# Kernel optimization log

Measured on AMD Instinct MI355X. Metric: run time of the kernel, lower is better.

## Reference

```python
import jax, jax.numpy as jnp
import numpy as np

P = 16; IMG = 800; GRID = IMG // P; NP = GRID * GRID  # 2500 patches
D = P * P * 3  # 768
H = 8; HD = D // H; FF = 2048; L = 2; B = 2
NM = NP // 2; NV = NP - NM  # 1250 / 1250


def _ln(x, g, b):
    m = x.mean(-1, keepdims=True)
    v = ((x - m) ** 2).mean(-1, keepdims=True)
    return (x - m) * jax.lax.rsqrt(v + 1e-5) * g + b


def _block(x, qkv_w, qkv_b, out_w, out_b, w1, b1, w2, b2, g1, be1, g2, be2):
    # pre-LN-free MAE block: attn -> add&norm -> FFN -> add&norm (dropout in eval = identity)
    Bb, N, _ = x.shape
    qkv = (x @ qkv_w + qkv_b).reshape(Bb, N, 3, H, HD)
    q, k, v = qkv[:, :, 0], qkv[:, :, 1], qkv[:, :, 2]  # [B,N,H,HD]
    scores = jnp.einsum('bnhd,bmhd->bhnm', q, k) / np.float32(np.sqrt(HD))
    w = jax.nn.softmax(scores, axis=-1)
    ao = jnp.einsum('bhnm,bmhd->bnhd', w, v).reshape(Bb, N, D) @ out_w + out_b
    x = _ln(x + ao, g1, be1)
    f = jax.nn.relu(x @ w1 + b1) @ w2 + b2
    return _ln(x + f, g2, be2)


def _patchify(x):
    Bb = x.shape[0]
    # torch unfold(2,P,P).unfold(3,P,P) -> [B,C,h,w,p,p] -> [B,h*w,C*p*p]
    return x.reshape(Bb, 3, GRID, P, GRID, P).transpose(0, 2, 4, 1, 3, 5).reshape(Bb, NP, D)


def setup_inputs() -> dict:
    key = jax.random.key(0)
    ks = jax.random.split(key, 32)
    inp = {}
    inp['x'] = jax.random.normal(ks[0], (B, 3, IMG, IMG), jnp.float32)
    perm = jax.vmap(lambda k: jax.random.permutation(k, NP))(jax.random.split(ks[1], B))
    inp['visible_idx'] = perm[:, NM:].astype(jnp.int32)  # perm order, like torch
    inp['masked_idx'] = perm[:, :NM].astype(jnp.int32)
    c = [2]
    def nx(shape, s=0.02):
        k = ks[c[0]]; c[0] += 1
        return jax.random.normal(k, shape, jnp.float32) * s
    for p in ['enc', 'dec']:
        inp[p + '_qkv_w'] = nx((L, D, 3 * D)); inp[p + '_qkv_b'] = jnp.zeros((L, 3 * D), jnp.float32)
        inp[p + '_out_w'] = nx((L, D, D));     inp[p + '_out_b'] = jnp.zeros((L, D), jnp.float32)
        inp[p + '_w1'] = nx((L, D, FF));       inp[p + '_b1'] = jnp.zeros((L, FF), jnp.float32)
        inp[p + '_w2'] = nx((L, FF, D));       inp[p + '_b2'] = jnp.zeros((L, D), jnp.float32)
        inp[p + '_g1'] = jnp.ones((L, D), jnp.float32);  inp[p + '_be1'] = jnp.zeros((L, D), jnp.float32)
        inp[p + '_g2'] = jnp.ones((L, D), jnp.float32);  inp[p + '_be2'] = jnp.zeros((L, D), jnp.float32)
    inp['out_w'] = nx((D, D)); inp['out_b'] = jnp.zeros((D,), jnp.float32)
    inp['mask_token'] = nx((D,))
    inp['enc_pos'] = nx((NV, D))
    inp['dec_pos'] = nx((NP, D))
    return inp


def reference(x, visible_idx, masked_idx,
              enc_qkv_w, enc_qkv_b, enc_out_w, enc_out_b, enc_w1, enc_b1, enc_w2, enc_b2,
              enc_g1, enc_be1, enc_g2, enc_be2,
              dec_qkv_w, dec_qkv_b, dec_out_w, dec_out_b, dec_w1, dec_b1, dec_w2, dec_b2,
              dec_g1, dec_be1, dec_g2, dec_be2,
              out_w, out_b, mask_token, enc_pos, dec_pos):
    patches = _patchify(x)                                    # [B,NP,D]
    b_ix = jnp.arange(B)[:, None]
    vis = patches[b_ix, visible_idx]                          # [B,NV,D] in perm order
    h = vis + enc_pos[None]
    for i in range(L):
        h = _block(h, enc_qkv_w[i], enc_qkv_b[i], enc_out_w[i], enc_out_b[i],
                   enc_w1[i], enc_b1[i], enc_w2[i], enc_b2[i],
                   enc_g1[i], enc_be1[i], enc_g2[i], enc_be2[i])
    # torch: full_sequence[mask==0] = visible_patches (row-major positions <- perm-order rows)
    vis_pos = jnp.sort(visible_idx, axis=1)
    full = jnp.broadcast_to(mask_token, (B, NP, D))           # masked positions = mask_token
    full = full.at[b_ix, vis_pos].set(h)
    h = full + dec_pos[None]
    for i in range(L):
        h = _block(h, dec_qkv_w[i], dec_qkv_b[i], dec_out_w[i], dec_out_b[i],
                   dec_w1[i], dec_b1[i], dec_w2[i], dec_b2[i],
                   dec_g1[i], dec_be1[i], dec_g2[i], dec_be2[i])
    return h @ out_w + out_b                                  # [B,NP,D]
```

## Files before the change

### kernel.cpp

```cpp
#include <hip/hip_runtime.h>
#include <cstdint>
#include <cstddef>


#define NBATCH  2
#define NPATCH  2500
#define NVIS    1250
#define DMODEL  768
#define NHEAD   8
#define HDIM    96
#define FFDIM   2048
#define NPADV   2560

typedef __attribute__((ext_vector_type(8))) short bf16x8;
typedef __attribute__((ext_vector_type(4))) float f32x4;

__device__ __forceinline__ short f2bf(float f){
  union { float f; unsigned u; } x; x.f = f;
  unsigned r = x.u + 0x7fffu + ((x.u >> 16) & 1u);
  return (short)(r >> 16);
}

__device__ __forceinline__ void async_copy16(void* lds, const void* g){
  __builtin_amdgcn_global_load_lds(
      (const __attribute__((address_space(1))) unsigned int*)g,
      (__attribute__((address_space(3))) unsigned int*)lds, 16, 0, 0);
}

struct TJob { const float* src; short* dst; int K; int N; int tile_base; int tiles_x; };
struct TJobs { TJob j[17]; };

__global__ __launch_bounds__(256) void transpose_all_kernel(TJobs jobs){
  int bid = blockIdx.x;
  int ji = 0;
  #pragma unroll
  for (int k=1;k<17;k++) if (bid >= jobs.j[k].tile_base) ji = k;
  TJob jb = jobs.j[ji];
  int lt = bid - jb.tile_base;
  int tx = lt % jb.tiles_x, ty = lt / jb.tiles_x;
  __shared__ float tile[32][33];
  int lx = threadIdx.x & 31, ly = threadIdx.x >> 5;
  #pragma unroll
  for (int r=0;r<4;r++)
    tile[ly + r*8][lx] = jb.src[(size_t)(ty*32 + ly + r*8)*jb.N + tx*32 + lx];
  __syncthreads();
  #pragma unroll
  for (int r=0;r<4;r++)
    jb.dst[(size_t)(tx*32 + ly + r*8)*jb.K + ty*32 + lx] = f2bf(tile[lx][ly + r*8]);
}

template<int MODE>
__global__ __launch_bounds__(256) void gemm_kernel(const short* __restrict__ A,
    const short* __restrict__ Wt, const float* __restrict__ bias,
    short* __restrict__ Cb, float* __restrict__ Cf, int M, int Nc, int K){
  __shared__ short ldsA[128*64];
  __shared__ short ldsB[128*64];
  const int t = threadIdx.x, w = t>>6, ln = t&63;
  const int m0 = blockIdx.x*128, n0 = blockIdx.y*128;
  const int wr = (w>>1)*64, wc = (w&1)*64;
  const f32x4 fz = {0.f,0.f,0.f,0.f};
  f32x4 acc[4][4];
  #pragma unroll
  for (int mi=0;mi<4;mi++)
    #pragma unroll
    for (int ni=0;ni<4;ni++) acc[mi][ni] = fz;
  const int nkt = K >> 6;
  for (int kt=0; kt<nkt; kt++){
    #pragma unroll
    for (int c=0;c<4;c++){
      int chunk = c*256 + t;
      int row = chunk>>3, seg = chunk&7, sgs = seg ^ (row&7);
      int gm = m0 + row; if (gm >= M) gm = M-1;
      async_copy16((char*)ldsA + c*4096 + w*1024, A  + (size_t)gm*K      + kt*64 + sgs*8);
      async_copy16((char*)ldsB + c*4096 + w*1024, Wt + (size_t)(n0+row)*K + kt*64 + sgs*8);
    }
    __syncthreads();
    #pragma unroll
    for (int ks=0;ks<2;ks++){
      bf16x8 af[4], bfr[4];
      #pragma unroll
      for (int mi=0;mi<4;mi++){
        int r = wr + mi*16 + (ln&15);
        int d = ks*4 + (ln>>4);
        af[mi]  = *(const bf16x8*)((const char*)ldsA + r*128 + ((d^(r&7))*16));
        int cc = wc + mi*16 + (ln&15);
        bfr[mi] = *(const bf16x8*)((const char*)ldsB + cc*128 + ((d^(cc&7))*16));
      }
      #pragma unroll
      for (int mi=0;mi<4;mi++)
        #pragma unroll
        for (int ni=0;ni<4;ni++)
          acc[mi][ni] = __builtin_amdgcn_mfma_f32_16x16x32_bf16(af[mi], bfr[ni], acc[mi][ni], 0,0,0);
    }
    __syncthreads();
  }
  float bv[4];
  #pragma unroll
  for (int ni=0;ni<4;ni++) bv[ni] = bias[n0 + wc + ni*16 + (ln&15)];
  #pragma unroll
  for (int mi=0;mi<4;mi++){
    #pragma unroll
    for (int j=0;j<4;j++){
      int gr = m0 + wr + mi*16 + (ln>>4)*4 + j;
      if (gr < M){
        #pragma unroll
        for (int ni=0;ni<4;ni++){
          float v = acc[mi][ni][j] + bv[ni];
          if (MODE==2) v = fmaxf(v, 0.f);
          int gc = n0 + wc + ni*16 + (ln&15);
          if (MODE==1) Cf[(size_t)gr*Nc + gc] = v;
          else         Cb[(size_t)gr*Nc + gc] = f2bf(v);
        }
      }
    }
  }
}

__global__ __launch_bounds__(256) void vtrans_kernel(const short* __restrict__ qkv,
    short* __restrict__ vt, int N){
  int bh = blockIdx.z;
  int b = bh >> 3, h = bh & 7;
  int n0 = blockIdx.x*32, hd0 = blockIdx.y*32;
  __shared__ short tile[32][33];
  int lx = threadIdx.x & 31, ly = threadIdx.x >> 5;
  #pragma unroll
  for (int r=0;r<4;r++){
    int n = n0 + ly + r*8;
    short val = 0;
    if (n < N) val = qkv[(size_t)(b*N+n)*2304 + 1536 + h*96 + hd0 + lx];
    tile[ly+r*8][lx] = val;
  }
  __syncthreads();
  #pragma unroll
  for (int r=0;r<4;r++){
    int hd = hd0 + ly + r*8, n = n0 + lx;
    vt[(size_t)(bh*96 + hd)*NPADV + n] = tile[lx][ly+r*8];
  }
}

__global__ __launch_bounds__(256) void attn_kernel(const short* __restrict__ qkv,
    const short* __restrict__ vt, short* __restrict__ ao, int N, int NT){
  __shared__ short Qs[64*104];
  __shared__ short Ks[64*104];
  __shared__ short Vs[96*72];
  __shared__ float Ps[4*16*68];
  const int t = threadIdx.x, w = t>>6, ln = t&63;
  const int bh = blockIdx.y, b = bh >> 3, h = bh & 7;
  const int q0 = blockIdx.x * 64;
  const float scale = 0.1020620726159658f;
  #pragma unroll
  for (int i=0;i<3;i++){
    int chunk = i*256 + t; int row = chunk/12, cs = chunk - row*12;
    int gn = q0 + row; if (gn >= N) gn = N-1;
    const short* gp = qkv + (size_t)(b*N+gn)*2304 + h*96 + cs*8;
    *(bf16x8*)&Qs[row*104 + cs*8] = *(const bf16x8*)gp;
  }
  __syncthreads();
  bf16x8 qf[3];
  #pragma unroll
  for (int ks=0;ks<3;ks++)
    qf[ks] = *(const bf16x8*)&Qs[(w*16 + (ln&15))*104 + (ks*4 + (ln>>4))*8];
  const f32x4 fz = {0.f,0.f,0.f,0.f};
  f32x4 o[6];
  #pragma unroll
  for (int g=0; g<6; g++) o[g] = fz;
  float mrun[4] = {-1e30f,-1e30f,-1e30f,-1e30f};
  float srun[4] = {0.f,0.f,0.f,0.f};
  for (int kt=0; kt<NT; kt++){
    int n0 = kt*64;
    #pragma unroll
    for (int i=0;i<3;i++){
      int chunk = i*256 + t; int row = chunk/12, cs = chunk - row*12;
      int gn = n0 + row; if (gn >= N) gn = N-1;
      const short* gp = qkv + (size_t)(b*N+gn)*2304 + 768 + h*96 + cs*8;
      *(bf16x8*)&Ks[row*104 + cs*8] = *(const bf16x8*)gp;
    }
    #pragma unroll
    for (int i=0;i<3;i++){
      int chunk = i*256 + t; int row = chunk>>3, seg = chunk&7;
      const short* gp = vt + (size_t)(bh*96 + row)*NPADV + n0 + seg*8;
      *(bf16x8*)&Vs[row*72 + seg*8] = *(const bf16x8*)gp;
    }
    __syncthreads();
    f32x4 s[4];
    #pragma unroll
    for (int tt=0;tt<4;tt++){
      f32x4 sc = fz;
      #pragma unroll
      for (int ks=0;ks<3;ks++){
        bf16x8 kb = *(const bf16x8*)&Ks[(tt*16 + (ln&15))*104 + (ks*4 + (ln>>4))*8];
        sc = __builtin_amdgcn_mfma_f32_16x16x32_bf16(qf[ks], kb, sc, 0,0,0);
      }
      int col = n0 + tt*16 + (ln&15);
      float msk = (col < N) ? 0.f : -1e30f;
      #pragma unroll
      for (int j=0;j<4;j++) s[tt][j] = sc[j]*scale + msk;
    }
    #pragma unroll
    for (int j=0;j<4;j++){
      float mx = fmaxf(fmaxf(s[0][j], s[1][j]), fmaxf(s[2][j], s[3][j]));
      #pragma unroll
      for (int d=1; d<16; d<<=1) mx = fmaxf(mx, __shfl_xor(mx, d));
      float mnew = fmaxf(mrun[j], mx);
      float alpha = __expf(mrun[j] - mnew);
      mrun[j] = mnew;
      float ps = 0.f;
      #pragma unroll
      for (int tt=0;tt<4;tt++){ float pv = __expf(s[tt][j] - mnew); s[tt][j] = pv; ps += pv; }
      #pragma unroll
      for (int d=1; d<16; d<<=1) ps += __shfl_xor(ps, d);
      srun[j] = srun[j]*alpha + ps;
      #pragma unroll
      for (int g=0; g<6; g++) o[g][j] *= alpha;
    }
    #pragma unroll
    for (int tt=0;tt<4;tt++)
      #pragma unroll
      for (int j=0;j<4;j++)
        Ps[(w*16 + (ln>>4)*4 + j)*68 + tt*16 + (ln&15)] = s[tt][j];
    #pragma unroll
    for (int ks2=0; ks2<2; ks2++){
      const float* pr = &Ps[(w*16 + (ln&15))*68 + ks2*32 + (ln>>4)*8];
      f32x4 p0 = *(const f32x4*)pr;
      f32x4 p1 = *(const f32x4*)(pr+4);
      bf16x8 pa;
      #pragma unroll
      for (int j=0;j<4;j++){ pa[j] = f2bf(p0[j]); pa[4+j] = f2bf(p1[j]); }
      #pragma unroll
      for (int g=0; g<6; g++){
        bf16x8 vb = *(const bf16x8*)&Vs[(g*16 + (ln&15))*72 + (ks2*4 + (ln>>4))*8];
        o[g] = __builtin_amdgcn_mfma_f32_16x16x32_bf16(pa, vb, o[g], 0,0,0);
      }
    }
    __syncthreads();
  }
  float inv[4];
  #pragma unroll
  for (int j=0;j<4;j++) inv[j] = 1.f / srun[j];
  #pragma unroll
  for (int g=0; g<6; g++)
    #pragma unroll
    for (int j=0;j<4;j++){
      int qr = q0 + w*16 + (ln>>4)*4 + j;
      if (qr < N)
        ao[(size_t)(b*N+qr)*768 + h*96 + g*16 + (ln&15)] = f2bf(o[g][j]*inv[j]);
    }
}

__global__ __launch_bounds__(256) void ln_kernel(const float* __restrict__ xin,
    const float* __restrict__ add, const float* __restrict__ g,
    const float* __restrict__ be, float* __restrict__ xo, short* __restrict__ xob){
  int row = blockIdx.x, t = threadIdx.x;
  float e[3]; float s = 0.f;
  #pragma unroll
  for (int k=0;k<3;k++){
    size_t off = (size_t)row*768 + t + k*256;
    e[k] = xin[off] + add[off]; s += e[k];
  }
  #pragma unroll
  for (int d=32; d; d>>=1) s += __shfl_xor(s, d);
  __shared__ float red[8];
  if ((t&63)==0) red[t>>6] = s;
  __syncthreads();
  float mean = (red[0]+red[1]+red[2]+red[3]) * (1.f/768.f);
  float vs = 0.f;
  #pragma unroll
  for (int k=0;k<3;k++){ float dd = e[k]-mean; vs += dd*dd; }
  #pragma unroll
  for (int d=32; d; d>>=1) vs += __shfl_xor(vs, d);
  if ((t&63)==0) red[4 + (t>>6)] = vs;
  __syncthreads();
  float rstd = rsqrtf((red[4]+red[5]+red[6]+red[7]) * (1.f/768.f) + 1e-5f);
  #pragma unroll
  for (int k=0;k<3;k++){
    int c = t + k*256;
    size_t off = (size_t)row*768 + c;
    float ov = (e[k]-mean)*rstd*g[c] + be[c];
    xo[off] = ov; xob[off] = f2bf(ov);
  }
}

__global__ __launch_bounds__(256) void patchify_kernel(const float* __restrict__ x,
    const int* __restrict__ vis, const float* __restrict__ enc_pos,
    float* __restrict__ xe, short* __restrict__ xeb){
  int b = blockIdx.y, i = blockIdx.x;
  int pidx = vis[b*NVIS + i];
  int gy = pidx / 50, gx = pidx - gy*50;
  #pragma unroll
  for (int k=0;k<3;k++){
    int d = threadIdx.x + k*256;
    int c = d >> 8, rr = d & 255, py = rr >> 4, px = rr & 15;
    float v = x[(((size_t)b*3 + c)*800 + gy*16 + py)*800 + gx*16 + px]
            + enc_pos[(size_t)i*768 + d];
    size_t off = (size_t)(b*NVIS + i)*768 + d;
    xe[off] = v; xeb[off] = f2bf(v);
  }
}

__global__ __launch_bounds__(256) void rank_kernel(const int* __restrict__ vis,
    int* __restrict__ rnk){
  int b = blockIdx.y; int i = blockIdx.x*256 + threadIdx.x;
  if (i >= NVIS) return;
  int p = vis[b*NVIS + i]; int c = 0;
  for (int j=0;j<NVIS;j++) c += (vis[b*NVIS + j] < p) ? 1 : 0;
  rnk[b*NVIS + i] = c;
}

__global__ __launch_bounds__(256) void dec_init_kernel(const float* __restrict__ mask_token,
    const float* __restrict__ dec_pos, float* __restrict__ xd, short* __restrict__ xdb){
  int row = blockIdx.x;
  int p = row % NPATCH;
  #pragma unroll
  for (int k=0;k<3;k++){
    int c = threadIdx.x + k*256;
    float v = mask_token[c] + dec_pos[(size_t)p*768 + c];
    size_t off = (size_t)row*768 + c;
    xd[off] = v; xdb[off] = f2bf(v);
  }
}

__global__ __launch_bounds__(256) void scatter_kernel(const int* __restrict__ vis,
    const int* __restrict__ rnk, const float* __restrict__ xe,
    const float* __restrict__ dec_pos, float* __restrict__ xd, short* __restrict__ xdb){
  int b = blockIdx.y, i = blockIdx.x;
  int p = vis[b*NVIS+i]; int r = rnk[b*NVIS+i];
  #pragma unroll
  for (int k=0;k<3;k++){
    int c = threadIdx.x + k*256;
    float v = xe[(size_t)(b*NVIS + r)*768 + c] + dec_pos[(size_t)p*768 + c];
    size_t off = (size_t)(b*NPATCH + p)*768 + c;
    xd[off] = v; xdb[off] = f2bf(v);
  }
}

static void run_block(hipStream_t stream, float* xf, short* xb, int M, int N, int NT,
                      const short* wqkvT, const float* qkv_b, const short* woutT,
                      const float* out_b, const short* w1T, const float* b1,
                      const short* w2T, const float* b2,
                      const float* g1, const float* be1, const float* g2, const float* be2,
                      short* qkvb, short* vt, short* aob, short* ffnb, float* tmp){
  int mt = (M + 127)/128;
  gemm_kernel<0><<<dim3(mt, 18), 256, 0, stream>>>(xb, wqkvT, qkv_b, qkvb, nullptr, M, 2304, 768);
  vtrans_kernel<<<dim3(NT*2, 3, 16), 256, 0, stream>>>(qkvb, vt, N);
  attn_kernel<<<dim3(NT, 16), 256, 0, stream>>>(qkvb, vt, aob, N, NT);
  gemm_kernel<1><<<dim3(mt, 6), 256, 0, stream>>>(aob, woutT, out_b, nullptr, tmp, M, 768, 768);
  ln_kernel<<<M, 256, 0, stream>>>(xf, tmp, g1, be1, xf, xb);
  gemm_kernel<2><<<dim3(mt, 16), 256, 0, stream>>>(xb, w1T, b1, ffnb, nullptr, M, 2048, 768);
  gemm_kernel<1><<<dim3(mt, 6), 256, 0, stream>>>(ffnb, w2T, b2, nullptr, tmp, M, 768, 2048);
  ln_kernel<<<M, 256, 0, stream>>>(xf, tmp, g2, be2, xf, xb);
}

extern "C" void kernel_launch(void* const* d_in, const int* in_sizes, int n_in,
                              void* d_out, int out_size, void* d_ws, size_t ws_size,
                              hipStream_t stream){
  const float* x        = (const float*)d_in[0];
  const int*   vis      = (const int*)d_in[1];
  const float* eqkv_w   = (const float*)d_in[3];
  const float* eqkv_b   = (const float*)d_in[4];
  const float* eout_w   = (const float*)d_in[5];
  const float* eout_b   = (const float*)d_in[6];
  const float* ew1      = (const float*)d_in[7];
  const float* eb1      = (const float*)d_in[8];
  const float* ew2      = (const float*)d_in[9];
  const float* eb2      = (const float*)d_in[10];
  const float* eg1      = (const float*)d_in[11];
  const float* ebe1     = (const float*)d_in[12];
  const float* eg2      = (const float*)d_in[13];
  const float* ebe2     = (const float*)d_in[14];
  const float* dqkv_w   = (const float*)d_in[15];
  const float* dqkv_b   = (const float*)d_in[16];
  const float* dout_w   = (const float*)d_in[17];
  const float* dout_b   = (const float*)d_in[18];
  const float* dw1      = (const float*)d_in[19];
  const float* db1      = (const float*)d_in[20];
  const float* dw2      = (const float*)d_in[21];
  const float* db2      = (const float*)d_in[22];
  const float* dg1      = (const float*)d_in[23];
  const float* dbe1     = (const float*)d_in[24];
  const float* dg2      = (const float*)d_in[25];
  const float* dbe2     = (const float*)d_in[26];
  const float* fout_w   = (const float*)d_in[27];
  const float* fout_b   = (const float*)d_in[28];
  const float* mask_tok = (const float*)d_in[29];
  const float* enc_posp = (const float*)d_in[30];
  const float* dec_posp = (const float*)d_in[31];

  char* p = (char*)d_ws;
  auto alloc = [&](size_t bytes)->char*{ char* r = p; p += (bytes + 255) & ~(size_t)255; return r; };

  const float* qkvw_s[2] = {eqkv_w, dqkv_w};
  const float* outw_s[2] = {eout_w, dout_w};
  const float* w1_s[2]   = {ew1, dw1};
  const float* w2_s[2]   = {ew2, dw2};

  short *wq[2][2], *wo[2][2], *w1t[2][2], *w2t[2][2];
  TJobs jobs; int jidx = 0; int tbase = 0;
  auto addJob = [&](const float* src, short* dst, int K, int N){
    jobs.j[jidx].src = src; jobs.j[jidx].dst = dst; jobs.j[jidx].K = K; jobs.j[jidx].N = N;
    jobs.j[jidx].tile_base = tbase; jobs.j[jidx].tiles_x = N/32;
    tbase += (K/32)*(N/32); jidx++;
  };
  for (int s=0;s<2;s++)
    for (int i=0;i<2;i++){
      wq[s][i]  = (short*)alloc((size_t)2304*768*2);
      addJob(qkvw_s[s] + (size_t)i*768*2304, wq[s][i], 768, 2304);
      wo[s][i]  = (short*)alloc((size_t)768*768*2);
      addJob(outw_s[s] + (size_t)i*768*768, wo[s][i], 768, 768);
      w1t[s][i] = (short*)alloc((size_t)2048*768*2);
      addJob(w1_s[s] + (size_t)i*768*2048, w1t[s][i], 768, 2048);
      w2t[s][i] = (short*)alloc((size_t)768*2048*2);
      addJob(w2_s[s] + (size_t)i*2048*768, w2t[s][i], 2048, 768);
    }
  short* wfin = (short*)alloc((size_t)768*768*2);
  addJob(fout_w, wfin, 768, 768);
  int total_tiles = tbase;

  float* xe   = (float*)alloc((size_t)2500*768*4);
  short* xeb  = (short*)alloc((size_t)2500*768*2);
  float* xd   = (float*)alloc((size_t)5000*768*4);
  short* xdb  = (short*)alloc((size_t)5000*768*2);
  short* qkvb = (short*)alloc((size_t)5000*2304*2);
  short* vt   = (short*)alloc((size_t)16*96*NPADV*2);
  short* aob  = (short*)alloc((size_t)5000*768*2);
  short* ffnb = (short*)alloc((size_t)5000*2048*2);
  float* tmp  = (float*)alloc((size_t)5000*768*4);
  int*   rnk  = (int*)alloc((size_t)2*NVIS*4);

  transpose_all_kernel<<<total_tiles, 256, 0, stream>>>(jobs);
  patchify_kernel<<<dim3(NVIS, NBATCH), 256, 0, stream>>>(x, vis, enc_posp, xe, xeb);
  rank_kernel<<<dim3((NVIS+255)/256, NBATCH), 256, 0, stream>>>(vis, rnk);

  for (int i=0;i<2;i++)
    run_block(stream, xe, xeb, 2500, 1250, 20,
              wq[0][i], eqkv_b + i*2304, wo[0][i], eout_b + i*768,
              w1t[0][i], eb1 + i*2048, w2t[0][i], eb2 + i*768,
              eg1 + i*768, ebe1 + i*768, eg2 + i*768, ebe2 + i*768,
              qkvb, vt, aob, ffnb, tmp);

  dec_init_kernel<<<NBATCH*NPATCH, 256, 0, stream>>>(mask_tok, dec_posp, xd, xdb);
  scatter_kernel<<<dim3(NVIS, NBATCH), 256, 0, stream>>>(vis, rnk, xe, dec_posp, xd, xdb);

  for (int i=0;i<2;i++)
    run_block(stream, xd, xdb, 5000, 2500, 40,
              wq[1][i], dqkv_b + i*2304, wo[1][i], dout_b + i*768,
              w1t[1][i], db1 + i*2048, w2t[1][i], db2 + i*768,
              dg1 + i*768, dbe1 + i*768, dg2 + i*768, dbe2 + i*768,
              qkvb, vt, aob, ffnb, tmp);

  gemm_kernel<1><<<dim3(40, 6), 256, 0, stream>>>(xdb, wfin, fout_b, nullptr,
                                                  (float*)d_out, 5000, 768, 768);
}
```

Before: 1.197 ms.

## Restructure attention kernel with async swizzled LDS loads and lazy softmax rescale

Rewrites the flash-attention inner loop. Q is loaded straight into registers, and K/V tiles are copied with async global-to-LDS copies into an XOR-swizzled layout to avoid bank conflicts. The softmax now uses exp2 with a folded log2e scale, rescales the running max only when it grows past a threshold, and defers the row-sum reduction to the end. P is stored as bf16 in a per-wave LDS region, and s_setprio is raised around the MFMA sections. Together these cut LDS traffic, conversions and shuffles per tile. The trade-offs are more complex indexing and reliance on the threshold trick staying numerically safe.

New measurement: 1.100 ms. 8.1% less time.

```diff
diff --git a/kernel.cpp b/kernel.cpp
--- a/kernel.cpp
+++ b/kernel.cpp
@@ -140,110 +140,130 @@
 
 __global__ __launch_bounds__(256) void attn_kernel(const short* __restrict__ qkv,
     const short* __restrict__ vt, short* __restrict__ ao, int N, int NT){
-  __shared__ short Qs[64*104];
-  __shared__ short Ks[64*104];
-  __shared__ short Vs[96*72];
-  __shared__ float Ps[4*16*68];
+  __shared__ short Ks[64*128];
+  __shared__ short Vs[96*64];
+  __shared__ short Ps[4*16*72];
   const int t = threadIdx.x, w = t>>6, ln = t&63;
+  const int col = ln & 15, hi = ln >> 4;
   const int bh = blockIdx.y, b = bh >> 3, h = bh & 7;
   const int q0 = blockIdx.x * 64;
-  const float scale = 0.1020620726159658f;
-  #pragma unroll
-  for (int i=0;i<3;i++){
-    int chunk = i*256 + t; int row = chunk/12, cs = chunk - row*12;
-    int gn = q0 + row; if (gn >= N) gn = N-1;
-    const short* gp = qkv + (size_t)(b*N+gn)*2304 + h*96 + cs*8;
-    *(bf16x8*)&Qs[row*104 + cs*8] = *(const bf16x8*)gp;
-  }
-  __syncthreads();
+  short* Pw = &Ps[w*16*72];
+  const float scale2 = 0.14724974f;
+
   bf16x8 qf[3];
-  #pragma unroll
-  for (int ks=0;ks<3;ks++)
-    qf[ks] = *(const bf16x8*)&Qs[(w*16 + (ln&15))*104 + (ks*4 + (ln>>4))*8];
+  {
+    int gq = q0 + w*16 + col; if (gq >= N) gq = N-1;
+    const short* qrow = qkv + (size_t)(b*N+gq)*2304 + h*96;
+    #pragma unroll
+    for (int ks=0;ks<3;ks++)
+      qf[ks] = *(const bf16x8*)(qrow + ks*32 + hi*8);
+  }
   const f32x4 fz = {0.f,0.f,0.f,0.f};
   f32x4 o[6];
   #pragma unroll
   for (int g=0; g<6; g++) o[g] = fz;
-  float mrun[4] = {-1e30f,-1e30f,-1e30f,-1e30f};
+  float mrun[4] = {-3e38f,-3e38f,-3e38f,-3e38f};
   float srun[4] = {0.f,0.f,0.f,0.f};
+
   for (int kt=0; kt<NT; kt++){
     int n0 = kt*64;
     #pragma unroll
+    for (int i=0;i<4;i++){
+      int chunk = i*256 + t, row = chunk>>4, seg = chunk&15;
+      int s2 = seg ^ (row&7);
+      int gn = n0 + row; if (gn >= N) gn = N-1;
+      const short* src = qkv + (size_t)(b*N+gn)*2304 + 768 + h*96
+                       + ((s2 < 12) ? s2*8 : 0);
+      async_copy16((char*)Ks + i*4096 + w*1024, src);
+    }
+    #pragma unroll
     for (int i=0;i<3;i++){
-      int chunk = i*256 + t; int row = chunk/12, cs = chunk - row*12;
-      int gn = n0 + row; if (gn >= N) gn = N-1;
-      const short* gp = qkv + (size_t)(b*N+gn)*2304 + 768 + h*96 + cs*8;
-      *(bf16x8*)&Ks[row*104 + cs*8] = *(const bf16x8*)gp;
-    }
-    #pragma unroll
-    for (int i=0;i<3;i++){
-      int chunk = i*256 + t; int row = chunk>>3, seg = chunk&7;
-      const short* gp = vt + (size_t)(bh*96 + row)*NPADV + n0 + seg*8;
-      *(bf16x8*)&Vs[row*72 + seg*8] = *(const bf16x8*)gp;
+      int chunk = i*256 + t, row = chunk>>3, seg = chunk&7;
+      int s2 = seg ^ (row&7);
+      const short* src = vt + (size_t)(bh*96 + row)*NPADV + n0 + s2*8;
+      async_copy16((char*)Vs + i*4096 + w*1024, src);
     }
     __syncthreads();
+
     f32x4 s[4];
+    __builtin_amdgcn_s_setprio(1);
     #pragma unroll
     for (int tt=0;tt<4;tt++){
       f32x4 sc = fz;
       #pragma unroll
       for (int ks=0;ks<3;ks++){
-        bf16x8 kb = *(const bf16x8*)&Ks[(tt*16 + (ln&15))*104 + (ks*4 + (ln>>4))*8];
+        int r = tt*16 + col, d = ks*4 + hi;
+        bf16x8 kb = *(const bf16x8*)((const char*)Ks + r*256 + ((d ^ (r&7))*16));
         sc = __builtin_amdgcn_mfma_f32_16x16x32_bf16(qf[ks], kb, sc, 0,0,0);
       }
-      int col = n0 + tt*16 + (ln&15);
-      float msk = (col < N) ? 0.f : -1e30f;
-      #pragma unroll
-      for (int j=0;j<4;j++) s[tt][j] = sc[j]*scale + msk;
-    }
+      s[tt] = sc;
+    }
+    __builtin_amdgcn_s_setprio(0);
+
+    #pragma unroll
+    for (int tt=0;tt<4;tt++){
+      float msk = (n0 + tt*16 + col < N) ? 0.f : -3e38f;
+      #pragma unroll
+      for (int j=0;j<4;j++) s[tt][j] = s[tt][j]*scale2 + msk;
+    }
+    float mx[4]; bool exc = false;
     #pragma unroll
     for (int j=0;j<4;j++){
-      float mx = fmaxf(fmaxf(s[0][j], s[1][j]), fmaxf(s[2][j], s[3][j]));
-      #pragma unroll
-      for (int d=1; d<16; d<<=1) mx = fmaxf(mx, __shfl_xor(mx, d));
-      float mnew = fmaxf(mrun[j], mx);
-      float alpha = __expf(mrun[j] - mnew);
-      mrun[j] = mnew;
+      float m0 = fmaxf(fmaxf(s[0][j], s[1][j]), fmaxf(s[2][j], s[3][j]));
+      #pragma unroll
+      for (int d=1; d<16; d<<=1) m0 = fmaxf(m0, __shfl_xor(m0, d));
+      mx[j] = m0;
+      exc = exc || (m0 > mrun[j] + 11.5f);
+    }
+    if (__any((int)exc)){
+      #pragma unroll
+      for (int j=0;j<4;j++){
+        float mnew = fmaxf(mrun[j], mx[j]);
+        float a = exp2f(mrun[j] - mnew);
+        mrun[j] = mnew; srun[j] *= a;
+        #pragma unroll
+        for (int g=0; g<6; g++) o[g][j] *= a;
+      }
+    }
+    #pragma unroll
+    for (int j=0;j<4;j++){
       float ps = 0.f;
       #pragma unroll
-      for (int tt=0;tt<4;tt++){ float pv = __expf(s[tt][j] - mnew); s[tt][j] = pv; ps += pv; }
-      #pragma unroll
-      for (int d=1; d<16; d<<=1) ps += __shfl_xor(ps, d);
-      srun[j] = srun[j]*alpha + ps;
-      #pragma unroll
-      for (int g=0; g<6; g++) o[g][j] *= alpha;
-    }
-    #pragma unroll
-    for (int tt=0;tt<4;tt++)
-      #pragma unroll
-      for (int j=0;j<4;j++)
-        Ps[(w*16 + (ln>>4)*4 + j)*68 + tt*16 + (ln&15)] = s[tt][j];
+      for (int tt=0;tt<4;tt++){ float pv = exp2f(s[tt][j] - mrun[j]); s[tt][j] = pv; ps += pv; }
+      srun[j] += ps;
+      #pragma unroll
+      for (int tt=0;tt<4;tt++)
+        Pw[(hi*4+j)*72 + tt*16 + col] = f2bf(s[tt][j]);
+    }
+    __builtin_amdgcn_s_setprio(1);
     #pragma unroll
     for (int ks2=0; ks2<2; ks2++){
-      const float* pr = &Ps[(w*16 + (ln&15))*68 + ks2*32 + (ln>>4)*8];
-      f32x4 p0 = *(const f32x4*)pr;
-      f32x4 p1 = *(const f32x4*)(pr+4);
-      bf16x8 pa;
-      #pragma unroll
-      for (int j=0;j<4;j++){ pa[j] = f2bf(p0[j]); pa[4+j] = f2bf(p1[j]); }
+      bf16x8 pa = *(const bf16x8*)&Pw[col*72 + (ks2*4 + hi)*8];
       #pragma unroll
       for (int g=0; g<6; g++){
-        bf16x8 vb = *(const bf16x8*)&Vs[(g*16 + (ln&15))*72 + (ks2*4 + (ln>>4))*8];
+        int r = g*16 + col, d = ks2*4 + hi;
+        bf16x8 vb = *(const bf16x8*)((const char*)Vs + r*128 + ((d ^ (r&7))*16));
         o[g] = __builtin_amdgcn_mfma_f32_16x16x32_bf16(pa, vb, o[g], 0,0,0);
       }
     }
+    __builtin_amdgcn_s_setprio(0);
     __syncthreads();
   }
   float inv[4];
   #pragma unroll
-  for (int j=0;j<4;j++) inv[j] = 1.f / srun[j];
+  for (int j=0;j<4;j++){
+    float ssum = srun[j];
+    #pragma unroll
+    for (int d=1; d<16; d<<=1) ssum += __shfl_xor(ssum, d);
+    inv[j] = 1.f / ssum;
+  }
   #pragma unroll
   for (int g=0; g<6; g++)
     #pragma unroll
     for (int j=0;j<4;j++){
-      int qr = q0 + w*16 + (ln>>4)*4 + j;
+      int qr = q0 + w*16 + hi*4 + j;
       if (qr < N)
-        ao[(size_t)(b*N+qr)*768 + h*96 + g*16 + (ln&15)] = f2bf(o[g][j]*inv[j]);
+        ao[(size_t)(b*N+qr)*768 + h*96 + g*16 + col] = f2bf(o[g][j]*inv[j]);
     }
 }
 
```
